# Kernel optimization log

Hardware: AMD Instinct MI355X
Metric: run time of the kernel (lower is better)

The kernel has to match this reference:

```python
import jax, jax.numpy as jnp
import numpy as np


def setup_inputs() -> dict:
    key = jax.random.key(0)
    k1, k2, k3, k4 = jax.random.split(key, 4)
    B, S, C = 16, 2048, 512
    x = jax.random.normal(k1, (B, S, C), dtype=jnp.float32)
    x_prime = jax.random.normal(k2, (B, S, C), dtype=jnp.float32)
    W = jax.random.normal(k3, (C, C), dtype=jnp.float32) * (1.0 / np.sqrt(C))
    b = jax.random.normal(k4, (C,), dtype=jnp.float32) * 0.01
    return {"x": x, "x_prime": x_prime, "W": W, "b": b}


def reference(x, x_prime, W, b):
    # q = Linear(x_prime): [B, S, C]
    q = jnp.einsum("bsc,dc->bsd", x_prime, W) + b
    # score = tanh(x_prime) @ q^T : [B, S, S]
    score = jnp.einsum("bsc,btc->bst", jnp.tanh(x_prime), q)
    alpha = jax.nn.softmax(score, axis=-1)
    # y_att = alpha @ x : [B, S, C]
    y_att = jnp.einsum("bst,btc->bsc", alpha, x)
    # dropout is identity in eval mode
    return jnp.tanh(y_att)
```

## Files before the change

### kernel.cpp

```cpp
#include <hip/hip_runtime.h>
#include <hip/hip_bf16.h>
#include <math.h>

typedef __bf16 bf16x8 __attribute__((ext_vector_type(8)));
typedef float  f32x4  __attribute__((ext_vector_type(4)));

#define MFMA16(a, b, c) __builtin_amdgcn_mfma_f32_16x16x32_bf16((a), (b), (c), 0, 0, 0)

static constexpr int    kB  = 16;
static constexpr int    kS  = 2048;
static constexpr int    kC  = 512;
static constexpr size_t kNE = (size_t)kB * kS * kC;

static __device__ __forceinline__ void split_bf16(float v, __bf16 &hi, __bf16 &lo) {
  hi = (__bf16)v;
  lo = (__bf16)(v - (float)hi);
}

static __device__ __forceinline__ void stage_split16(
    const float* __restrict__ src, __bf16* hi, __bf16* lo, int o) {
  float4 v0 = *(const float4*)(src + 0);
  float4 v1 = *(const float4*)(src + 4);
  float4 v2 = *(const float4*)(src + 8);
  float4 v3 = *(const float4*)(src + 12);
  float vv[16] = {v0.x, v0.y, v0.z, v0.w, v1.x, v1.y, v1.z, v1.w,
                  v2.x, v2.y, v2.z, v2.w, v3.x, v3.y, v3.z, v3.w};
  bf16x8 h0, h1, l0, l1;
#pragma unroll
  for (int i = 0; i < 8; ++i) {
    __bf16 a, b;
    split_bf16(vv[i], a, b);     h0[i] = a; l0[i] = b;
    split_bf16(vv[8 + i], a, b); h1[i] = a; l1[i] = b;
  }
  *(bf16x8*)&hi[o]     = h0;
  *(bf16x8*)&hi[o + 8] = h1;
  *(bf16x8*)&lo[o]     = l0;
  *(bf16x8*)&lo[o + 8] = l1;
}

__global__ __launch_bounds__(256) void k_tanh_split(
    const float* __restrict__ xp, __bf16* __restrict__ th, __bf16* __restrict__ tl) {
  size_t i = ((size_t)blockIdx.x * 256 + threadIdx.x) * 8;
  float4 a = *(const float4*)(xp + i);
  float4 b = *(const float4*)(xp + i + 4);
  float v[8] = {a.x, a.y, a.z, a.w, b.x, b.y, b.z, b.w};
  bf16x8 h, l;
#pragma unroll
  for (int k = 0; k < 8; ++k) {
    float t = tanhf(v[k]);
    __bf16 hh, ll;
    split_bf16(t, hh, ll);
    h[k] = hh; l[k] = ll;
  }
  *(bf16x8*)(th + i) = h;
  *(bf16x8*)(tl + i) = l;
}

__global__ __launch_bounds__(256) void k_transpose_x(
    const float* __restrict__ x, __bf16* __restrict__ xbt) {
  __shared__ float tile[64][65];
  int bid = blockIdx.x;
  int b   = bid >> 8;
  int t0  = ((bid >> 3) & 31) * 64;
  int c0  = (bid & 7) * 64;
  int row = threadIdx.x >> 2;
  int seg = threadIdx.x & 3;
  const float* src = x + (size_t)(b * kS + t0 + row) * kC + c0 + seg * 16;
  float4 v0 = *(const float4*)(src + 0);
  float4 v1 = *(const float4*)(src + 4);
  float4 v2 = *(const float4*)(src + 8);
  float4 v3 = *(const float4*)(src + 12);
  float vv[16] = {v0.x, v0.y, v0.z, v0.w, v1.x, v1.y, v1.z, v1.w,
                  v2.x, v2.y, v2.z, v2.w, v3.x, v3.y, v3.z, v3.w};
#pragma unroll
  for (int i = 0; i < 16; ++i) tile[row][seg * 16 + i] = vv[i];
  __syncthreads();
  bf16x8 o0, o1;
#pragma unroll
  for (int i = 0; i < 8; ++i) o0[i] = (__bf16)tile[seg * 16 + i][row];
#pragma unroll
  for (int i = 0; i < 8; ++i) o1[i] = (__bf16)tile[seg * 16 + 8 + i][row];
  __bf16* dst = xbt + (size_t)(b * kC + c0 + row) * kS + t0 + seg * 16;
  *(bf16x8*)(dst)     = o0;
  *(bf16x8*)(dst + 8) = o1;
}

__global__ __launch_bounds__(256) void k_qgemm(
    const float* __restrict__ xp, const float* __restrict__ W,
    const float* __restrict__ bias, __bf16* __restrict__ qh, __bf16* __restrict__ ql) {
  __shared__ __align__(16) __bf16 lds[4 * 4608];
  __bf16* Ah = lds;
  __bf16* Al = lds + 4608;
  __bf16* Bh = lds + 9216;
  __bf16* Bl = lds + 13824;

  int bid = blockIdx.x;
  int n0  = (bid & 7) * 64;
  int m0  = (bid >> 3) * 64;

  int tid  = threadIdx.x;
  int lane = tid & 63;
  int wave = tid >> 6;
  int qd   = lane >> 4;
  int cl   = lane & 15;
  int row  = tid >> 2;
  int seg  = tid & 3;

  f32x4 acc[4] = {};

  for (int kc = 0; kc < 8; ++kc) {
    stage_split16(xp + (size_t)(m0 + row) * kC + kc * 64 + seg * 16, Ah, Al, row * 72 + seg * 16);
    stage_split16(W  + (size_t)(n0 + row) * kC + kc * 64 + seg * 16, Bh, Bl, row * 72 + seg * 16);
    __syncthreads();
#pragma unroll
    for (int ks = 0; ks < 2; ++ks) {
      int ka = ks * 32 + qd * 8;
      bf16x8 ah = *(const bf16x8*)&Ah[(wave * 16 + cl) * 72 + ka];
      bf16x8 al = *(const bf16x8*)&Al[(wave * 16 + cl) * 72 + ka];
#pragma unroll
      for (int j = 0; j < 4; ++j) {
        bf16x8 bh = *(const bf16x8*)&Bh[(j * 16 + cl) * 72 + ka];
        bf16x8 bl = *(const bf16x8*)&Bl[(j * 16 + cl) * 72 + ka];
        acc[j] = MFMA16(ah, bh, acc[j]);
        acc[j] = MFMA16(ah, bl, acc[j]);
        acc[j] = MFMA16(al, bh, acc[j]);
      }
    }
    __syncthreads();
  }
#pragma unroll
  for (int j = 0; j < 4; ++j) {
    int d = n0 + j * 16 + cl;
    float bv = bias[d];
#pragma unroll
    for (int r = 0; r < 4; ++r) {
      int m = m0 + wave * 16 + qd * 4 + r;
      float v = acc[j][r] + bv;
      __bf16 h, l;
      split_bf16(v, h, l);
      qh[(size_t)m * kC + d] = h;
      ql[(size_t)m * kC + d] = l;
    }
  }
}

__global__ __launch_bounds__(256, 2) void k_attn(
    const __bf16* __restrict__ th, const __bf16* __restrict__ tl,
    const __bf16* __restrict__ qh, const __bf16* __restrict__ ql,
    const __bf16* __restrict__ xbt, float* __restrict__ out) {
  __shared__ __align__(16) __bf16 lds[27648];
  __bf16* Ah = lds;
  __bf16* Al = lds + 4608;
  __bf16* Bh = lds + 9216;
  __bf16* Bl = lds + 18432;
  __bf16* P  = lds;
  __bf16* Xt = lds + 9216;

  int bid = blockIdx.x;
  int b   = (bid & 7) | ((bid >> 8) << 3);
  int s0  = ((bid >> 3) & 31) * 64;

  int tid  = threadIdx.x;
  int lane = tid & 63;
  int wave = tid >> 6;
  int qd   = lane >> 4;
  int cl   = lane & 15;

  const float LOG2E = 1.4426950408889634f;

  float m_r[4], l_r[4];
  f32x4 O[8][4] = {};
#pragma unroll
  for (int r = 0; r < 4; ++r) { m_r[r] = -INFINITY; l_r[r] = 0.f; }

  const size_t rowbase = (size_t)b * kS;

  for (int tt = 0; tt < 16; ++tt) {
    int t0 = tt * 128;
    f32x4 Sacc[8] = {};
    for (int kc = 0; kc < 8; ++kc) {
      {
        int arow = tid >> 2, aseg = tid & 3;
        size_t g = (rowbase + s0 + arow) * kC + kc * 64 + aseg * 16;
        int o = arow * 72 + aseg * 16;
        *(bf16x8*)&Ah[o]     = *(const bf16x8*)(th + g);
        *(bf16x8*)&Ah[o + 8] = *(const bf16x8*)(th + g + 8);
        *(bf16x8*)&Al[o]     = *(const bf16x8*)(tl + g);
        *(bf16x8*)&Al[o + 8] = *(const bf16x8*)(tl + g + 8);
      }
      {
        int brow = tid >> 1, bseg = tid & 1;
        size_t g = (rowbase + t0 + brow) * kC + kc * 64 + bseg * 32;
        int o = brow * 72 + bseg * 32;
#pragma unroll
        for (int u = 0; u < 4; ++u)
          *(bf16x8*)&Bh[o + u * 8] = *(const bf16x8*)(qh + g + u * 8);
#pragma unroll
        for (int u = 0; u < 4; ++u)
          *(bf16x8*)&Bl[o + u * 8] = *(const bf16x8*)(ql + g + u * 8);
      }
      __syncthreads();
#pragma unroll
      for (int ks = 0; ks < 2; ++ks) {
        int ka = ks * 32 + qd * 8;
        bf16x8 ah = *(const bf16x8*)&Ah[(wave * 16 + cl) * 72 + ka];
        bf16x8 al = *(const bf16x8*)&Al[(wave * 16 + cl) * 72 + ka];
#pragma unroll
        for (int j = 0; j < 8; ++j) {
          bf16x8 bh = *(const bf16x8*)&Bh[(j * 16 + cl) * 72 + ka];
          bf16x8 bl = *(const bf16x8*)&Bl[(j * 16 + cl) * 72 + ka];
          Sacc[j] = MFMA16(ah, bh, Sacc[j]);
          Sacc[j] = MFMA16(ah, bl, Sacc[j]);
          Sacc[j] = MFMA16(al, bh, Sacc[j]);
        }
      }
      __syncthreads();
    }
    float rmax[4];
#pragma unroll
    for (int r = 0; r < 4; ++r) {
      float v = Sacc[0][r];
#pragma unroll
      for (int j = 1; j < 8; ++j) v = fmaxf(v, Sacc[j][r]);
      rmax[r] = v;
    }
#pragma unroll
    for (int mk = 1; mk < 16; mk <<= 1)
#pragma unroll
      for (int r = 0; r < 4; ++r)
        rmax[r] = fmaxf(rmax[r], __shfl_xor(rmax[r], mk, 64));
    float alpha[4], rsum[4];
#pragma unroll
    for (int r = 0; r < 4; ++r) {
      float mn = fmaxf(m_r[r], rmax[r]);
      alpha[r] = exp2f((m_r[r] - mn) * LOG2E);
      m_r[r] = mn;
      rsum[r] = 0.f;
    }
#pragma unroll
    for (int j = 0; j < 8; ++j)
#pragma unroll
      for (int r = 0; r < 4; ++r) {
        float p = exp2f((Sacc[j][r] - m_r[r]) * LOG2E);
        Sacc[j][r] = p;
        rsum[r] += p;
      }
#pragma unroll
    for (int mk = 1; mk < 16; mk <<= 1)
#pragma unroll
      for (int r = 0; r < 4; ++r)
        rsum[r] += __shfl_xor(rsum[r], mk, 64);
    f32x4 av;
#pragma unroll
    for (int r = 0; r < 4; ++r) {
      l_r[r] = l_r[r] * alpha[r] + rsum[r];
      av[r] = alpha[r];
    }
#pragma unroll
    for (int nc = 0; nc < 8; ++nc)
#pragma unroll
      for (int nt = 0; nt < 4; ++nt)
        O[nc][nt] *= av;
#pragma unroll
    for (int j = 0; j < 8; ++j)
#pragma unroll
      for (int r = 0; r < 4; ++r)
        P[(wave * 16 + qd * 4 + r) * 136 + j * 16 + cl] = (__bf16)Sacc[j][r];
    __syncthreads();
#pragma unroll
    for (int nc = 0; nc < 8; ++nc) {
      {
        int xrow = tid >> 2, xseg = tid & 3;
        size_t g = ((size_t)b * kC + nc * 64 + xrow) * kS + t0 + xseg * 32;
        int o = xrow * 136 + xseg * 32;
#pragma unroll
        for (int u = 0; u < 4; ++u)
          *(bf16x8*)&Xt[o + u * 8] = *(const bf16x8*)(xbt + g + u * 8);
      }
      __syncthreads();
#pragma unroll
      for (int ks = 0; ks < 4; ++ks) {
        int ka = ks * 32 + qd * 8;
        bf16x8 pa = *(const bf16x8*)&P[(wave * 16 + cl) * 136 + ka];
#pragma unroll
        for (int nt = 0; nt < 4; ++nt) {
          bf16x8 xb = *(const bf16x8*)&Xt[(nt * 16 + cl) * 136 + ka];
          O[nc][nt] = MFMA16(pa, xb, O[nc][nt]);
        }
      }
      __syncthreads();
    }
  }
#pragma unroll
  for (int r = 0; r < 4; ++r) {
    float inv = __builtin_amdgcn_rcpf(l_r[r]);
    size_t rowoff = (rowbase + s0 + wave * 16 + qd * 4 + r) * kC;
#pragma unroll
    for (int nc = 0; nc < 8; ++nc)
#pragma unroll
      for (int nt = 0; nt < 4; ++nt) {
        float v = O[nc][nt][r] * inv;
        float e = exp2f(2.f * LOG2E * v);
        out[rowoff + nc * 64 + nt * 16 + cl] = 1.f - 2.f * __builtin_amdgcn_rcpf(e + 1.f);
      }
  }
}

extern "C" void kernel_launch(void* const* d_in, const int* in_sizes, int n_in,
                              void* d_out, int out_size, void* d_ws, size_t ws_size,
                              hipStream_t stream) {
  const float* x    = (const float*)d_in[0];
  const float* xp   = (const float*)d_in[1];
  const float* W    = (const float*)d_in[2];
  const float* bias = (const float*)d_in[3];
  float* out = (float*)d_out;

  __bf16* ws  = (__bf16*)d_ws;
  __bf16* th  = ws;
  __bf16* tl  = ws + kNE;
  __bf16* qh  = ws + 2 * kNE;
  __bf16* ql  = ws + 3 * kNE;
  __bf16* xbt = ws + 4 * kNE;

  k_tanh_split<<<8192, 256, 0, stream>>>(xp, th, tl);
  k_transpose_x<<<4096, 256, 0, stream>>>(x, xbt);
  k_qgemm<<<4096, 256, 0, stream>>>(xp, W, bias, qh, ql);
  k_attn<<<512, 256, 0, stream>>>(th, tl, qh, ql, xbt, out);
}
```

Before: 1.003 ms.

## Prefetch next tiles into registers and XOR-swizzle LDS in qgemm and attention

Both the q GEMM and the attention kernel now load the next K-chunk or X tile from global memory into registers while the current tile is being multiplied, so global latency overlaps the MFMA work. The padded LDS layout (row stride 72/136) is replaced by a dense, XOR-swizzled layout to avoid bank conflicts. P fragments are hoisted into registers once per tile, and s_setprio is raised around the MFMA loops. The cost is more live registers per thread, which risks spills or lower occupancy under launch_bounds(256,2). LDS use also grows to 48KB in the attention kernel.

```diff
diff --git a/kernel.cpp b/kernel.cpp
--- a/kernel.cpp
+++ b/kernel.cpp
@@ -17,12 +17,15 @@
   lo = (__bf16)(v - (float)hi);
 }
 
-static __device__ __forceinline__ void stage_split16(
-    const float* __restrict__ src, __bf16* hi, __bf16* lo, int o) {
-  float4 v0 = *(const float4*)(src + 0);
-  float4 v1 = *(const float4*)(src + 4);
-  float4 v2 = *(const float4*)(src + 8);
-  float4 v3 = *(const float4*)(src + 12);
+static __device__ __forceinline__ int swzb(int row, int e) {
+  return ((row << 7) + (e << 1)) ^ ((row & 7) << 4);
+}
+static __device__ __forceinline__ int swzp(int row, int e) {
+  return ((row << 8) + (e << 1)) ^ ((row & 7) << 4);
+}
+
+static __device__ __forceinline__ void split_store16_swz(
+    float4 v0, float4 v1, float4 v2, float4 v3, char* hi, char* lo, int row, int e0) {
   float vv[16] = {v0.x, v0.y, v0.z, v0.w, v1.x, v1.y, v1.z, v1.w,
                   v2.x, v2.y, v2.z, v2.w, v3.x, v3.y, v3.z, v3.w};
   bf16x8 h0, h1, l0, l1;
@@ -32,10 +35,10 @@
     split_bf16(vv[i], a, b);     h0[i] = a; l0[i] = b;
     split_bf16(vv[8 + i], a, b); h1[i] = a; l1[i] = b;
   }
-  *(bf16x8*)&hi[o]     = h0;
-  *(bf16x8*)&hi[o + 8] = h1;
-  *(bf16x8*)&lo[o]     = l0;
-  *(bf16x8*)&lo[o + 8] = l1;
+  *(bf16x8*)(hi + swzb(row, e0))     = h0;
+  *(bf16x8*)(hi + swzb(row, e0 + 8)) = h1;
+  *(bf16x8*)(lo + swzb(row, e0))     = l0;
+  *(bf16x8*)(lo + swzb(row, e0 + 8)) = l1;
 }
 
 __global__ __launch_bounds__(256) void k_tanh_split(
@@ -88,11 +91,11 @@
 __global__ __launch_bounds__(256) void k_qgemm(
     const float* __restrict__ xp, const float* __restrict__ W,
     const float* __restrict__ bias, __bf16* __restrict__ qh, __bf16* __restrict__ ql) {
-  __shared__ __align__(16) __bf16 lds[4 * 4608];
-  __bf16* Ah = lds;
-  __bf16* Al = lds + 4608;
-  __bf16* Bh = lds + 9216;
-  __bf16* Bl = lds + 13824;
+  __shared__ __align__(16) char lds[32768];
+  char* Ah = lds;
+  char* Al = lds + 8192;
+  char* Bh = lds + 16384;
+  char* Bl = lds + 24576;
 
   int bid = blockIdx.x;
   int n0  = (bid & 7) * 64;
@@ -107,25 +110,41 @@
   int seg  = tid & 3;
 
   f32x4 acc[4] = {};
-
+  const float* srcA = xp + (size_t)(m0 + row) * kC + seg * 16;
+  const float* srcB = W  + (size_t)(n0 + row) * kC + seg * 16;
+
+  float4 va0, va1, va2, va3, vb0, vb1, vb2, vb3;
+  auto load_ab = [&](int kc) {
+    const float* a = srcA + kc * 64;
+    va0 = *(const float4*)(a);      va1 = *(const float4*)(a + 4);
+    va2 = *(const float4*)(a + 8);  va3 = *(const float4*)(a + 12);
+    const float* bb = srcB + kc * 64;
+    vb0 = *(const float4*)(bb);     vb1 = *(const float4*)(bb + 4);
+    vb2 = *(const float4*)(bb + 8); vb3 = *(const float4*)(bb + 12);
+  };
+
+  load_ab(0);
   for (int kc = 0; kc < 8; ++kc) {
-    stage_split16(xp + (size_t)(m0 + row) * kC + kc * 64 + seg * 16, Ah, Al, row * 72 + seg * 16);
-    stage_split16(W  + (size_t)(n0 + row) * kC + kc * 64 + seg * 16, Bh, Bl, row * 72 + seg * 16);
+    split_store16_swz(va0, va1, va2, va3, Ah, Al, row, seg * 16);
+    split_store16_swz(vb0, vb1, vb2, vb3, Bh, Bl, row, seg * 16);
     __syncthreads();
+    if (kc < 7) load_ab(kc + 1);
+    __builtin_amdgcn_s_setprio(1);
 #pragma unroll
     for (int ks = 0; ks < 2; ++ks) {
       int ka = ks * 32 + qd * 8;
-      bf16x8 ah = *(const bf16x8*)&Ah[(wave * 16 + cl) * 72 + ka];
-      bf16x8 al = *(const bf16x8*)&Al[(wave * 16 + cl) * 72 + ka];
+      bf16x8 ah = *(const bf16x8*)(Ah + swzb(wave * 16 + cl, ka));
+      bf16x8 al = *(const bf16x8*)(Al + swzb(wave * 16 + cl, ka));
 #pragma unroll
       for (int j = 0; j < 4; ++j) {
-        bf16x8 bh = *(const bf16x8*)&Bh[(j * 16 + cl) * 72 + ka];
-        bf16x8 bl = *(const bf16x8*)&Bl[(j * 16 + cl) * 72 + ka];
+        bf16x8 bh = *(const bf16x8*)(Bh + swzb(j * 16 + cl, ka));
+        bf16x8 bl = *(const bf16x8*)(Bl + swzb(j * 16 + cl, ka));
         acc[j] = MFMA16(ah, bh, acc[j]);
         acc[j] = MFMA16(ah, bl, acc[j]);
         acc[j] = MFMA16(al, bh, acc[j]);
       }
     }
+    __builtin_amdgcn_s_setprio(0);
     __syncthreads();
   }
 #pragma unroll
@@ -148,13 +167,13 @@
     const __bf16* __restrict__ th, const __bf16* __restrict__ tl,
     const __bf16* __restrict__ qh, const __bf16* __restrict__ ql,
     const __bf16* __restrict__ xbt, float* __restrict__ out) {
-  __shared__ __align__(16) __bf16 lds[27648];
-  __bf16* Ah = lds;
-  __bf16* Al = lds + 4608;
-  __bf16* Bh = lds + 9216;
-  __bf16* Bl = lds + 18432;
-  __bf16* P  = lds;
-  __bf16* Xt = lds + 9216;
+  __shared__ __align__(16) char lds[49152];
+  char* Ah = lds;
+  char* Al = lds + 8192;
+  char* Bh = lds + 16384;
+  char* Bl = lds + 32768;
+  char* P  = lds;
+  char* Xt = lds + 16384;
 
   int bid = blockIdx.x;
   int b   = (bid & 7) | ((bid >> 8) << 3);
@@ -175,47 +194,68 @@
 
   const size_t rowbase = (size_t)b * kS;
 
+  const int arow = tid >> 2, aseg = tid & 3;
+  const int brow = tid >> 1, bseg = tid & 1;
+  const int xrow = tid >> 2, xseg = tid & 3;
+
+  bf16x8 rah[2], ral[2], rbh[4], rbl[4], rx[4], pa[4];
+
+  auto load_a = [&](int kc) {
+    size_t g = (rowbase + s0 + arow) * kC + kc * 64 + aseg * 16;
+    rah[0] = *(const bf16x8*)(th + g); rah[1] = *(const bf16x8*)(th + g + 8);
+    ral[0] = *(const bf16x8*)(tl + g); ral[1] = *(const bf16x8*)(tl + g + 8);
+  };
+  auto load_b = [&](int kc, int t0q) {
+    size_t g = (rowbase + t0q + brow) * kC + kc * 64 + bseg * 32;
+#pragma unroll
+    for (int u = 0; u < 4; ++u) {
+      rbh[u] = *(const bf16x8*)(qh + g + u * 8);
+      rbl[u] = *(const bf16x8*)(ql + g + u * 8);
+    }
+  };
+  auto load_x = [&](int nc, int t0q) {
+    size_t g = ((size_t)b * kC + nc * 64 + xrow) * kS + t0q + xseg * 32;
+#pragma unroll
+    for (int u = 0; u < 4; ++u) rx[u] = *(const bf16x8*)(xbt + g + u * 8);
+  };
+
+  load_a(0);
+  load_b(0, 0);
+
   for (int tt = 0; tt < 16; ++tt) {
     int t0 = tt * 128;
     f32x4 Sacc[8] = {};
     for (int kc = 0; kc < 8; ++kc) {
-      {
-        int arow = tid >> 2, aseg = tid & 3;
-        size_t g = (rowbase + s0 + arow) * kC + kc * 64 + aseg * 16;
-        int o = arow * 72 + aseg * 16;
-        *(bf16x8*)&Ah[o]     = *(const bf16x8*)(th + g);
-        *(bf16x8*)&Ah[o + 8] = *(const bf16x8*)(th + g + 8);
-        *(bf16x8*)&Al[o]     = *(const bf16x8*)(tl + g);
-        *(bf16x8*)&Al[o + 8] = *(const bf16x8*)(tl + g + 8);
-      }
-      {
-        int brow = tid >> 1, bseg = tid & 1;
-        size_t g = (rowbase + t0 + brow) * kC + kc * 64 + bseg * 32;
-        int o = brow * 72 + bseg * 32;
-#pragma unroll
-        for (int u = 0; u < 4; ++u)
-          *(bf16x8*)&Bh[o + u * 8] = *(const bf16x8*)(qh + g + u * 8);
-#pragma unroll
-        for (int u = 0; u < 4; ++u)
-          *(bf16x8*)&Bl[o + u * 8] = *(const bf16x8*)(ql + g + u * 8);
+      *(bf16x8*)(Ah + swzb(arow, aseg * 16))     = rah[0];
+      *(bf16x8*)(Ah + swzb(arow, aseg * 16 + 8)) = rah[1];
+      *(bf16x8*)(Al + swzb(arow, aseg * 16))     = ral[0];
+      *(bf16x8*)(Al + swzb(arow, aseg * 16 + 8)) = ral[1];
+#pragma unroll
+      for (int u = 0; u < 4; ++u) {
+        *(bf16x8*)(Bh + swzb(brow, bseg * 32 + u * 8)) = rbh[u];
+        *(bf16x8*)(Bl + swzb(brow, bseg * 32 + u * 8)) = rbl[u];
       }
       __syncthreads();
+      if (kc < 7) { load_a(kc + 1); load_b(kc + 1, t0); }
+      __builtin_amdgcn_s_setprio(1);
 #pragma unroll
       for (int ks = 0; ks < 2; ++ks) {
         int ka = ks * 32 + qd * 8;
-        bf16x8 ah = *(const bf16x8*)&Ah[(wave * 16 + cl) * 72 + ka];
-        bf16x8 al = *(const bf16x8*)&Al[(wave * 16 + cl) * 72 + ka];
+        bf16x8 ah = *(const bf16x8*)(Ah + swzb(wave * 16 + cl, ka));
+        bf16x8 al = *(const bf16x8*)(Al + swzb(wave * 16 + cl, ka));
 #pragma unroll
         for (int j = 0; j < 8; ++j) {
-          bf16x8 bh = *(const bf16x8*)&Bh[(j * 16 + cl) * 72 + ka];
-          bf16x8 bl = *(const bf16x8*)&Bl[(j * 16 + cl) * 72 + ka];
+          bf16x8 bh = *(const bf16x8*)(Bh + swzb(j * 16 + cl, ka));
+          bf16x8 bl = *(const bf16x8*)(Bl + swzb(j * 16 + cl, ka));
           Sacc[j] = MFMA16(ah, bh, Sacc[j]);
           Sacc[j] = MFMA16(ah, bl, Sacc[j]);
           Sacc[j] = MFMA16(al, bh, Sacc[j]);
         }
       }
+      __builtin_amdgcn_s_setprio(0);
       __syncthreads();
     }
+    load_x(0, t0);
     float rmax[4];
 #pragma unroll
     for (int r = 0; r < 4; ++r) {
@@ -264,30 +304,39 @@
 #pragma unroll
     for (int j = 0; j < 8; ++j)
 #pragma unroll
-      for (int r = 0; r < 4; ++r)
-        P[(wave * 16 + qd * 4 + r) * 136 + j * 16 + cl] = (__bf16)Sacc[j][r];
-    __syncthreads();
+      for (int r = 0; r < 4; ++r) {
+        int prow = wave * 16 + qd * 4 + r;
+        int off  = ((prow << 8) + ((j * 16 + cl) << 1)) ^ ((prow & 7) << 4);
+        *(__bf16*)(P + off) = (__bf16)Sacc[j][r];
+      }
 #pragma unroll
     for (int nc = 0; nc < 8; ++nc) {
-      {
-        int xrow = tid >> 2, xseg = tid & 3;
-        size_t g = ((size_t)b * kC + nc * 64 + xrow) * kS + t0 + xseg * 32;
-        int o = xrow * 136 + xseg * 32;
-#pragma unroll
-        for (int u = 0; u < 4; ++u)
-          *(bf16x8*)&Xt[o + u * 8] = *(const bf16x8*)(xbt + g + u * 8);
-      }
+#pragma unroll
+      for (int u = 0; u < 4; ++u)
+        *(bf16x8*)(Xt + swzp(xrow, xseg * 32 + u * 8)) = rx[u];
       __syncthreads();
+      if (nc == 0) {
+#pragma unroll
+        for (int ks = 0; ks < 4; ++ks)
+          pa[ks] = *(const bf16x8*)(P + swzp(wave * 16 + cl, ks * 32 + qd * 8));
+      }
+      if (nc < 7) {
+        load_x(nc + 1, t0);
+      } else if (tt < 15) {
+        load_a(0);
+        load_b(0, t0 + 128);
+      }
+      __builtin_amdgcn_s_setprio(1);
 #pragma unroll
       for (int ks = 0; ks < 4; ++ks) {
         int ka = ks * 32 + qd * 8;
-        bf16x8 pa = *(const bf16x8*)&P[(wave * 16 + cl) * 136 + ka];
 #pragma unroll
         for (int nt = 0; nt < 4; ++nt) {
-          bf16x8 xb = *(const bf16x8*)&Xt[(nt * 16 + cl) * 136 + ka];
-          O[nc][nt] = MFMA16(pa, xb, O[nc][nt]);
+          bf16x8 xb = *(const bf16x8*)(Xt + swzp(nt * 16 + cl, ka));
+          O[nc][nt] = MFMA16(pa[ks], xb, O[nc][nt]);
         }
       }
+      __builtin_amdgcn_s_setprio(0);
       __syncthreads();
     }
   }
```

New measurement: 1.069 ms. 6.7% more time.

## Retile attention to 32-row blocks with split-column waves and async LDS loads

Applied to the files above, without the earlier changes.

The attention kernel now processes 32 query rows per block instead of 64 and launches twice as many blocks. Each wave owns a 16-row by 64-key slice of the score tile and half of the output channels, and the waves exchange row max and row sum through LDS. Q tiles are loaded directly into LDS with global_load_lds using an XOR swizzle, and s_setprio raises wave priority around the MFMA loops; occupancy is raised to 3 blocks per CU. This is meant to improve CU occupancy and load balance on the chip, at the cost of extra barriers, re-reading the tanh tiles for more blocks, and loading both X halves in every step.

```diff
diff --git a/kernel.cpp b/kernel.cpp
--- a/kernel.cpp
+++ b/kernel.cpp
@@ -17,25 +17,10 @@
   lo = (__bf16)(v - (float)hi);
 }
 
-static __device__ __forceinline__ void stage_split16(
-    const float* __restrict__ src, __bf16* hi, __bf16* lo, int o) {
-  float4 v0 = *(const float4*)(src + 0);
-  float4 v1 = *(const float4*)(src + 4);
-  float4 v2 = *(const float4*)(src + 8);
-  float4 v3 = *(const float4*)(src + 12);
-  float vv[16] = {v0.x, v0.y, v0.z, v0.w, v1.x, v1.y, v1.z, v1.w,
-                  v2.x, v2.y, v2.z, v2.w, v3.x, v3.y, v3.z, v3.w};
-  bf16x8 h0, h1, l0, l1;
-#pragma unroll
-  for (int i = 0; i < 8; ++i) {
-    __bf16 a, b;
-    split_bf16(vv[i], a, b);     h0[i] = a; l0[i] = b;
-    split_bf16(vv[8 + i], a, b); h1[i] = a; l1[i] = b;
-  }
-  *(bf16x8*)&hi[o]     = h0;
-  *(bf16x8*)&hi[o + 8] = h1;
-  *(bf16x8*)&lo[o]     = l0;
-  *(bf16x8*)&lo[o + 8] = l1;
+static __device__ __forceinline__ void gload16(const void* g, void* l) {
+  __builtin_amdgcn_global_load_lds(
+      (const __attribute__((address_space(1))) char*)g,
+      (__attribute__((address_space(3))) char*)l, 16, 0, 0);
 }
 
 __global__ __launch_bounds__(256) void k_tanh_split(
@@ -108,10 +93,31 @@
 
   f32x4 acc[4] = {};
 
+  auto stage16 = [&](const float* src, __bf16* hi, __bf16* lo, int o) {
+    float4 v0 = *(const float4*)(src + 0);
+    float4 v1 = *(const float4*)(src + 4);
+    float4 v2 = *(const float4*)(src + 8);
+    float4 v3 = *(const float4*)(src + 12);
+    float vv[16] = {v0.x, v0.y, v0.z, v0.w, v1.x, v1.y, v1.z, v1.w,
+                    v2.x, v2.y, v2.z, v2.w, v3.x, v3.y, v3.z, v3.w};
+    bf16x8 h0, h1, l0, l1;
+#pragma unroll
+    for (int i = 0; i < 8; ++i) {
+      __bf16 a, b;
+      split_bf16(vv[i], a, b);     h0[i] = a; l0[i] = b;
+      split_bf16(vv[8 + i], a, b); h1[i] = a; l1[i] = b;
+    }
+    *(bf16x8*)&hi[o]     = h0;
+    *(bf16x8*)&hi[o + 8] = h1;
+    *(bf16x8*)&lo[o]     = l0;
+    *(bf16x8*)&lo[o + 8] = l1;
+  };
+
   for (int kc = 0; kc < 8; ++kc) {
-    stage_split16(xp + (size_t)(m0 + row) * kC + kc * 64 + seg * 16, Ah, Al, row * 72 + seg * 16);
-    stage_split16(W  + (size_t)(n0 + row) * kC + kc * 64 + seg * 16, Bh, Bl, row * 72 + seg * 16);
+    stage16(xp + (size_t)(m0 + row) * kC + kc * 64 + seg * 16, Ah, Al, row * 72 + seg * 16);
+    stage16(W  + (size_t)(n0 + row) * kC + kc * 64 + seg * 16, Bh, Bl, row * 72 + seg * 16);
     __syncthreads();
+    __builtin_amdgcn_s_setprio(1);
 #pragma unroll
     for (int ks = 0; ks < 2; ++ks) {
       int ka = ks * 32 + qd * 8;
@@ -126,6 +132,7 @@
         acc[j] = MFMA16(al, bh, acc[j]);
       }
     }
+    __builtin_amdgcn_s_setprio(0);
     __syncthreads();
   }
 #pragma unroll
@@ -144,76 +151,86 @@
   }
 }
 
-__global__ __launch_bounds__(256, 2) void k_attn(
+__global__ __launch_bounds__(256, 3) void k_attn(
     const __bf16* __restrict__ th, const __bf16* __restrict__ tl,
     const __bf16* __restrict__ qh, const __bf16* __restrict__ ql,
     const __bf16* __restrict__ xbt, float* __restrict__ out) {
-  __shared__ __align__(16) __bf16 lds[27648];
-  __bf16* Ah = lds;
-  __bf16* Al = lds + 4608;
-  __bf16* Bh = lds + 9216;
-  __bf16* Bl = lds + 18432;
-  __bf16* P  = lds;
-  __bf16* Xt = lds + 9216;
+  __shared__ __align__(16) char lds[44544];
+  float*  statm = (float*)lds;
+  float*  stats = (float*)(lds + 256);
+  __bf16* Ah    = (__bf16*)(lds + 512);
+  __bf16* Al    = (__bf16*)(lds + 5120);
+  char*   Bh    = lds + 9728;
+  char*   Bl    = lds + 26112;
+  __bf16* P     = (__bf16*)(lds + 512);
+  __bf16* Xt0   = (__bf16*)(lds + 9728);
+  __bf16* Xt1   = (__bf16*)(lds + 27136);
 
   int bid = blockIdx.x;
-  int b   = (bid & 7) | ((bid >> 8) << 3);
-  int s0  = ((bid >> 3) & 31) * 64;
+  int swz = (bid & 7) * 128 + (bid >> 3);
+  int b   = swz >> 6;
+  int s0  = (swz & 63) * 32;
 
   int tid  = threadIdx.x;
   int lane = tid & 63;
-  int wave = tid >> 6;
+  int wv   = tid >> 6;
   int qd   = lane >> 4;
   int cl   = lane & 15;
+  int rg   = wv & 1;
+  int cg   = wv >> 1;
 
   const float LOG2E = 1.4426950408889634f;
 
   float m_r[4], l_r[4];
-  f32x4 O[8][4] = {};
 #pragma unroll
   for (int r = 0; r < 4; ++r) { m_r[r] = -INFINITY; l_r[r] = 0.f; }
-
-  const size_t rowbase = (size_t)b * kS;
+  f32x4 O[4][4] = {};
+
+  auto stage_score = [&](int kc, int t0q) {
+    {
+      int ar = tid >> 3, as = tid & 7;
+      size_t g = (size_t)(b * kS + s0 + ar) * kC + kc * 64 + as * 8;
+      int o = ar * 72 + as * 8;
+      *(bf16x8*)&Ah[o] = *(const bf16x8*)(th + g);
+      *(bf16x8*)&Al[o] = *(const bf16x8*)(tl + g);
+    }
+#pragma unroll
+    for (int u = 0; u < 4; ++u) {
+      int slot = wv * 256 + u * 64 + lane;
+      int r = slot >> 3;
+      int c = (slot & 7) ^ (r & 7);
+      size_t g = (size_t)(b * kS + t0q + r) * kC + kc * 64 + c * 8;
+      int ldoff = (wv * 256 + u * 64) * 16;
+      gload16(qh + g, Bh + ldoff);
+      gload16(ql + g, Bl + ldoff);
+    }
+  };
 
   for (int tt = 0; tt < 16; ++tt) {
     int t0 = tt * 128;
-    f32x4 Sacc[8] = {};
+    f32x4 Sacc[4] = {};
     for (int kc = 0; kc < 8; ++kc) {
-      {
-        int arow = tid >> 2, aseg = tid & 3;
-        size_t g = (rowbase + s0 + arow) * kC + kc * 64 + aseg * 16;
-        int o = arow * 72 + aseg * 16;
-        *(bf16x8*)&Ah[o]     = *(const bf16x8*)(th + g);
-        *(bf16x8*)&Ah[o + 8] = *(const bf16x8*)(th + g + 8);
-        *(bf16x8*)&Al[o]     = *(const bf16x8*)(tl + g);
-        *(bf16x8*)&Al[o + 8] = *(const bf16x8*)(tl + g + 8);
-      }
-      {
-        int brow = tid >> 1, bseg = tid & 1;
-        size_t g = (rowbase + t0 + brow) * kC + kc * 64 + bseg * 32;
-        int o = brow * 72 + bseg * 32;
-#pragma unroll
-        for (int u = 0; u < 4; ++u)
-          *(bf16x8*)&Bh[o + u * 8] = *(const bf16x8*)(qh + g + u * 8);
-#pragma unroll
-        for (int u = 0; u < 4; ++u)
-          *(bf16x8*)&Bl[o + u * 8] = *(const bf16x8*)(ql + g + u * 8);
-      }
+      stage_score(kc, t0);
       __syncthreads();
+      __builtin_amdgcn_s_setprio(1);
 #pragma unroll
       for (int ks = 0; ks < 2; ++ks) {
         int ka = ks * 32 + qd * 8;
-        bf16x8 ah = *(const bf16x8*)&Ah[(wave * 16 + cl) * 72 + ka];
-        bf16x8 al = *(const bf16x8*)&Al[(wave * 16 + cl) * 72 + ka];
-#pragma unroll
-        for (int j = 0; j < 8; ++j) {
-          bf16x8 bh = *(const bf16x8*)&Bh[(j * 16 + cl) * 72 + ka];
-          bf16x8 bl = *(const bf16x8*)&Bl[(j * 16 + cl) * 72 + ka];
+        bf16x8 ah = *(const bf16x8*)&Ah[(rg * 16 + cl) * 72 + ka];
+        bf16x8 al = *(const bf16x8*)&Al[(rg * 16 + cl) * 72 + ka];
+        int kchunk = ks * 4 + qd;
+#pragma unroll
+        for (int j = 0; j < 4; ++j) {
+          int trow = cg * 64 + j * 16 + cl;
+          int boff = trow * 128 + ((kchunk ^ (trow & 7)) << 4);
+          bf16x8 bh = *(const bf16x8*)(Bh + boff);
+          bf16x8 bl = *(const bf16x8*)(Bl + boff);
           Sacc[j] = MFMA16(ah, bh, Sacc[j]);
           Sacc[j] = MFMA16(ah, bl, Sacc[j]);
           Sacc[j] = MFMA16(al, bh, Sacc[j]);
         }
       }
+      __builtin_amdgcn_s_setprio(0);
       __syncthreads();
     }
     float rmax[4];
@@ -221,7 +238,7 @@
     for (int r = 0; r < 4; ++r) {
       float v = Sacc[0][r];
 #pragma unroll
-      for (int j = 1; j < 8; ++j) v = fmaxf(v, Sacc[j][r]);
+      for (int j = 1; j < 4; ++j) v = fmaxf(v, Sacc[j][r]);
       rmax[r] = v;
     }
 #pragma unroll
@@ -229,16 +246,23 @@
 #pragma unroll
       for (int r = 0; r < 4; ++r)
         rmax[r] = fmaxf(rmax[r], __shfl_xor(rmax[r], mk, 64));
+    if (cl == 0) {
+#pragma unroll
+      for (int r = 0; r < 4; ++r)
+        statm[cg * 32 + rg * 16 + qd * 4 + r] = rmax[r];
+    }
+    __syncthreads();
     float alpha[4], rsum[4];
 #pragma unroll
     for (int r = 0; r < 4; ++r) {
-      float mn = fmaxf(m_r[r], rmax[r]);
-      alpha[r] = exp2f((m_r[r] - mn) * LOG2E);
-      m_r[r] = mn;
+      float om = statm[(cg ^ 1) * 32 + rg * 16 + qd * 4 + r];
+      float M  = fmaxf(m_r[r], fmaxf(rmax[r], om));
+      alpha[r] = exp2f((m_r[r] - M) * LOG2E);
+      m_r[r] = M;
       rsum[r] = 0.f;
     }
 #pragma unroll
-    for (int j = 0; j < 8; ++j)
+    for (int j = 0; j < 4; ++j)
 #pragma unroll
       for (int r = 0; r < 4; ++r) {
         float p = exp2f((Sacc[j][r] - m_r[r]) * LOG2E);
@@ -250,58 +274,73 @@
 #pragma unroll
       for (int r = 0; r < 4; ++r)
         rsum[r] += __shfl_xor(rsum[r], mk, 64);
+    if (cl == 0) {
+#pragma unroll
+      for (int r = 0; r < 4; ++r)
+        stats[cg * 32 + rg * 16 + qd * 4 + r] = rsum[r];
+    }
+#pragma unroll
+    for (int j = 0; j < 4; ++j)
+#pragma unroll
+      for (int r = 0; r < 4; ++r)
+        P[(rg * 16 + qd * 4 + r) * 136 + cg * 64 + j * 16 + cl] = (__bf16)Sacc[j][r];
     f32x4 av;
 #pragma unroll
-    for (int r = 0; r < 4; ++r) {
-      l_r[r] = l_r[r] * alpha[r] + rsum[r];
-      av[r] = alpha[r];
-    }
-#pragma unroll
-    for (int nc = 0; nc < 8; ++nc)
+    for (int r = 0; r < 4; ++r) av[r] = alpha[r];
+#pragma unroll
+    for (int st = 0; st < 4; ++st)
 #pragma unroll
       for (int nt = 0; nt < 4; ++nt)
-        O[nc][nt] *= av;
-#pragma unroll
-    for (int j = 0; j < 8; ++j)
-#pragma unroll
-      for (int r = 0; r < 4; ++r)
-        P[(wave * 16 + qd * 4 + r) * 136 + j * 16 + cl] = (__bf16)Sacc[j][r];
+        O[st][nt] *= av;
     __syncthreads();
 #pragma unroll
-    for (int nc = 0; nc < 8; ++nc) {
+    for (int r = 0; r < 4; ++r)
+      l_r[r] = l_r[r] * alpha[r] + rsum[r] + stats[(cg ^ 1) * 32 + rg * 16 + qd * 4 + r];
+    bf16x8 pa[4];
+#pragma unroll
+    for (int ks = 0; ks < 4; ++ks)
+      pa[ks] = *(const bf16x8*)&P[(rg * 16 + cl) * 136 + ks * 32 + qd * 8];
+#pragma unroll
+    for (int step = 0; step < 4; ++step) {
       {
-        int xrow = tid >> 2, xseg = tid & 3;
-        size_t g = ((size_t)b * kC + nc * 64 + xrow) * kS + t0 + xseg * 32;
-        int o = xrow * 136 + xseg * 32;
+        int xr = tid >> 2, xs = tid & 3;
+        size_t g0 = ((size_t)b * kC + step * 64 + xr) * kS + t0 + xs * 32;
+        size_t g1 = g0 + (size_t)256 * kS;
+        int o = xr * 136 + xs * 32;
 #pragma unroll
         for (int u = 0; u < 4; ++u)
-          *(bf16x8*)&Xt[o + u * 8] = *(const bf16x8*)(xbt + g + u * 8);
+          *(bf16x8*)&Xt0[o + u * 8] = *(const bf16x8*)(xbt + g0 + u * 8);
+#pragma unroll
+        for (int u = 0; u < 4; ++u)
+          *(bf16x8*)&Xt1[o + u * 8] = *(const bf16x8*)(xbt + g1 + u * 8);
       }
       __syncthreads();
+      const __bf16* Xt = cg ? Xt1 : Xt0;
+      __builtin_amdgcn_s_setprio(1);
 #pragma unroll
       for (int ks = 0; ks < 4; ++ks) {
         int ka = ks * 32 + qd * 8;
-        bf16x8 pa = *(const bf16x8*)&P[(wave * 16 + cl) * 136 + ka];
 #pragma unroll
         for (int nt = 0; nt < 4; ++nt) {
           bf16x8 xb = *(const bf16x8*)&Xt[(nt * 16 + cl) * 136 + ka];
-          O[nc][nt] = MFMA16(pa, xb, O[nc][nt]);
+          O[step][nt] = MFMA16(pa[ks], xb, O[step][nt]);
         }
       }
+      __builtin_amdgcn_s_setprio(0);
       __syncthreads();
     }
   }
 #pragma unroll
   for (int r = 0; r < 4; ++r) {
     float inv = __builtin_amdgcn_rcpf(l_r[r]);
-    size_t rowoff = (rowbase + s0 + wave * 16 + qd * 4 + r) * kC;
-#pragma unroll
-    for (int nc = 0; nc < 8; ++nc)
+    size_t rowoff = (size_t)(b * kS + s0 + rg * 16 + qd * 4 + r) * kC + cg * 256;
+#pragma unroll
+    for (int st = 0; st < 4; ++st)
 #pragma unroll
       for (int nt = 0; nt < 4; ++nt) {
-        float v = O[nc][nt][r] * inv;
+        float v = O[st][nt][r] * inv;
         float e = exp2f(2.f * LOG2E * v);
-        out[rowoff + nc * 64 + nt * 16 + cl] = 1.f - 2.f * __builtin_amdgcn_rcpf(e + 1.f);
+        out[rowoff + st * 64 + nt * 16 + cl] = 1.f - 2.f * __builtin_amdgcn_rcpf(e + 1.f);
       }
   }
 }
@@ -325,5 +364,5 @@
   k_tanh_split<<<8192, 256, 0, stream>>>(xp, th, tl);
   k_transpose_x<<<4096, 256, 0, stream>>>(x, xbt);
   k_qgemm<<<4096, 256, 0, stream>>>(xp, W, bias, qh, ql);
-  k_attn<<<512, 256, 0, stream>>>(th, tl, qh, ql, xbt, out);
-}
+  k_attn<<<1024, 256, 0, stream>>>(th, tl, qh, ql, xbt, out);
+}
```

After: 900.4 us. 10.2% less time.
